# Kernel tuning notes

Measured on AMD Instinct MI355X. Metric: run time of the kernel, lower is better.

The kernel has to match this reference:

```python
import jax, jax.numpy as jnp
import numpy as np

B, T, C = 4, 1024, 768
E, K = 8, 2               # n_exp, top_k
N = B * T                 # num_tokens
# eval-mode capacity: floor(K * eval_capacity(2.0) * N / E), rounded even, >= min_capacity(4)
CAP = 2048


def setup_inputs() -> dict:
    key = jax.random.key(0)
    k0, k1, k2, k3 = jax.random.split(key, 4)
    s = 0.02
    return {
        "x": jax.random.normal(k0, (B, T, C), jnp.float32),
        "w_g": jax.random.normal(k1, (E, C), jnp.float32) * s,
        "c_fc": jax.random.normal(k2, (E, C, 4 * C), jnp.float32) * s,
        "fc_bias": jnp.zeros((E, 1, 4 * C), jnp.float32),
        "c_proj": jax.random.normal(k3, (E, 4 * C, C), jnp.float32) * s,
        "proj_bias": jnp.zeros((E, 1, C), jnp.float32),
    }


def reference(x, w_g, c_fc, fc_bias, c_proj, proj_bias):
    xf = x.reshape(N, C)
    # ---- Router ----
    logits = xf @ w_g.T                                        # [N, E]
    top_v, top_i = jax.lax.top_k(logits, K)                    # [N, K]
    rows = jnp.arange(N)[:, None]
    masked = jnp.full((N, E), -jnp.inf, logits.dtype).at[rows, top_i].set(top_v)
    probs = jax.nn.softmax(masked, axis=-1)                    # [N, E] (zero off top-k)
    exp_mask = jax.nn.one_hot(top_i, E, dtype=jnp.float32)     # [N, K, E]
    exp_mask = exp_mask.transpose(1, 0, 2)                     # [K, N, E]
    # position of each assignment within its expert queue (top-1 assignments first)
    rank = jnp.cumsum(exp_mask.reshape(K * N, E), axis=0) - 1.0
    rank = rank.reshape(K, N, E)
    exp_mask = exp_mask * (rank < CAP)                         # drop over-capacity tokens
    rank_id = jnp.sum(exp_mask * rank, axis=-1).astype(jnp.int32)  # [K, N]
    exp_w = exp_mask * probs[None]                             # [K, N, E]
    rank_sc = jax.nn.one_hot(rank_id, CAP, dtype=jnp.float32)  # [K, N, CAP]
    cb_weight = jnp.einsum('kne,knc->nec', exp_w, rank_sc)     # [N, E, CAP] combine weights
    sec_mask = (cb_weight != 0).astype(xf.dtype)               # [N, E, CAP] dispatch mask
    # ---- Dispatch + batched experts (per-expert MLP via bmm) ----
    exp_in = jnp.einsum('nec,nd->ecd', sec_mask, xf)           # [E, CAP, C]
    h = jax.nn.gelu(jnp.einsum('ecd,edf->ecf', exp_in, c_fc) + fc_bias, approximate=False)
    exp_out = jnp.einsum('ecf,efd->ecd', h, c_proj) + proj_bias  # [E, CAP, C]
    # ---- Combine ----
    out = jnp.einsum('nec,ecd->nd', cb_weight, exp_out)        # [N, C]
    return out.reshape(B, T, C)
```

## Files before the change

### kernel.cpp

```cpp
#include <hip/hip_runtime.h>
#include <hip/hip_bf16.h>
#include <math.h>

#define N_TOK 4096
#define CDIM  768
#define E_EXP 8
#define CAPC  2048
#define HDIM  3072

typedef __attribute__((ext_vector_type(8))) short short8;
typedef __attribute__((ext_vector_type(4))) float floatx4;

#define VMCNT(n) asm volatile("s_waitcnt vmcnt(" #n ")" ::: "memory")
#define LGKM(n)  asm volatile("s_waitcnt lgkmcnt(" #n ")" ::: "memory")
#define SB0()    __builtin_amdgcn_sched_barrier(0)

static __device__ __forceinline__ unsigned short f2bf(float f) {
  __hip_bfloat16 h = __float2bfloat16(f);
  return __builtin_bit_cast(unsigned short, h);
}
static __device__ __forceinline__ float bf2f(unsigned short u) {
  return __builtin_bit_cast(float, (unsigned int)u << 16);
}

__device__ __forceinline__ void transpose_body(const float* __restrict__ ie,
                                               unsigned short* __restrict__ oe,
                                               int R, int Cc, int c0, int r0,
                                               float (*tile)[65])
{
  const int t = threadIdx.x;
  {
    const int r = t >> 2, c = (t & 3) * 4;
#pragma unroll
    for (int i = 0; i < 4; ++i) {
      const float4 v = *(const float4*)(ie + (size_t)(r0 + r) * Cc + c0 + c + i * 16);
      tile[r][c + i * 16 + 0] = v.x; tile[r][c + i * 16 + 1] = v.y;
      tile[r][c + i * 16 + 2] = v.z; tile[r][c + i * 16 + 3] = v.w;
    }
  }
  __syncthreads();
  {
    const int cc = t >> 2, rq = (t & 3) * 16;
    unsigned short o[16];
#pragma unroll
    for (int i = 0; i < 16; ++i) o[i] = f2bf(tile[rq + i][cc]);
    unsigned short* dst = oe + (size_t)(c0 + cc) * R + r0 + rq;
    *(short8*)(dst)     = *(short8*)&o[0];
    *(short8*)(dst + 8) = *(short8*)&o[8];
  }
}

__global__ __launch_bounds__(256)
void prep_kernel(const float* __restrict__ cfc, const float* __restrict__ cpr,
                 __hip_bfloat16* __restrict__ wfcT, __hip_bfloat16* __restrict__ wprT,
                 const float* __restrict__ x, const float* __restrict__ wg,
                 int* __restrict__ eidx, float* __restrict__ pval)
{
  __shared__ float tile[64][65];
  const int b = blockIdx.x;
  if (b < 4608) {
    const int e = b / (48 * 12), rem = b % (48 * 12);
    const int c0 = (rem % 48) * 64, r0 = (rem / 48) * 64;
    transpose_body(cfc + (size_t)e * CDIM * HDIM,
                   (unsigned short*)wfcT + (size_t)e * HDIM * CDIM,
                   CDIM, HDIM, c0, r0, tile);
  } else if (b < 9216) {
    const int bb = b - 4608;
    const int e = bb / (12 * 48), rem = bb % (12 * 48);
    const int c0 = (rem % 12) * 64, r0 = (rem / 12) * 64;
    transpose_body(cpr + (size_t)e * HDIM * CDIM,
                   (unsigned short*)wprT + (size_t)e * CDIM * HDIM,
                   HDIM, CDIM, c0, r0, tile);
  } else {
    const int wv = threadIdx.x >> 6, lane = threadIdx.x & 63;
    const int n = (b - 9216) * 4 + wv;
    const float* xr = x + (size_t)n * CDIM;
    float acc[E_EXP] = {0.f, 0.f, 0.f, 0.f, 0.f, 0.f, 0.f, 0.f};
#pragma unroll
    for (int i = 0; i < CDIM / 64; ++i) {
      const float xv = xr[i * 64 + lane];
#pragma unroll
      for (int e = 0; e < E_EXP; ++e)
        acc[e] = fmaf(xv, wg[e * CDIM + i * 64 + lane], acc[e]);
    }
#pragma unroll
    for (int e = 0; e < E_EXP; ++e) {
#pragma unroll
      for (int off = 32; off > 0; off >>= 1)
        acc[e] += __shfl_xor(acc[e], off);
    }
    if (lane == 0) {
      int e0 = 0; float v0 = acc[0];
#pragma unroll
      for (int e = 1; e < E_EXP; ++e) if (acc[e] > v0) { v0 = acc[e]; e0 = e; }
      int e1 = -1; float v1 = -3.4e38f;
#pragma unroll
      for (int e = 0; e < E_EXP; ++e) if (e != e0 && acc[e] > v1) { v1 = acc[e]; e1 = e; }
      const float ex = __expf(v1 - v0);
      const float inv = 1.f / (1.f + ex);
      eidx[n] = e0; eidx[N_TOK + n] = e1;
      pval[n] = inv; pval[N_TOK + n] = ex * inv;
    }
  }
}

__global__ __launch_bounds__(256)
void scan_kernel(const int* __restrict__ eidx, int* __restrict__ slot,
                 int* __restrict__ slot_token, int* __restrict__ ecnt,
                 int* __restrict__ work2, int* __restrict__ wcnt)
{
  const int t = threadIdx.x;
  const int base = t * 32;
  int e_local[32];
  int cnt[E_EXP] = {0, 0, 0, 0, 0, 0, 0, 0};
#pragma unroll
  for (int i = 0; i < 32; ++i) {
    const int e = eidx[base + i];
    e_local[i] = e;
    cnt[e]++;
  }
  __shared__ int hist[256][E_EXP];
  __shared__ int secnt[E_EXP];
#pragma unroll
  for (int e = 0; e < E_EXP; ++e) hist[t][e] = cnt[e];
  __syncthreads();
  for (int off = 1; off < 256; off <<= 1) {
    int v[E_EXP] = {0, 0, 0, 0, 0, 0, 0, 0};
    if (t >= off) {
#pragma unroll
      for (int e = 0; e < E_EXP; ++e) v[e] = hist[t - off][e];
    }
    __syncthreads();
    if (t >= off) {
#pragma unroll
      for (int e = 0; e < E_EXP; ++e) hist[t][e] += v[e];
    }
    __syncthreads();
  }
  if (t == 255) {
#pragma unroll
    for (int e = 0; e < E_EXP; ++e) {
      const int tot = hist[255][e];
      const int c = tot < CAPC ? tot : CAPC;
      ecnt[e] = c;
      secnt[e] = c;
    }
  }
  __syncthreads();
  if (t == 0) {
    int n2 = 0;
    for (int e = 0; e < E_EXP; ++e) {
      const int c = secnt[e];
      const int t2 = (c + 127) >> 7;
      for (int b = 0; b < t2; ++b) work2[n2++] = (e << 8) | b;
    }
    wcnt[0] = n2 * 24;
    wcnt[1] = n2 * 6;
  }
  int run[E_EXP];
#pragma unroll
  for (int e = 0; e < E_EXP; ++e) run[e] = hist[t][e] - cnt[e];
#pragma unroll
  for (int i = 0; i < 32; ++i) {
    const int a = base + i;
    const int e = e_local[i];
    const int r = run[e]++;
    const int s = (r < CAPC) ? r : -1;
    slot[a] = s;
    if (s >= 0) slot_token[e * CAPC + s] = (a < N_TOK) ? a : (a - N_TOK);
  }
}

__global__ __launch_bounds__(256)
void dispatch_kernel(const float* __restrict__ x, const int* __restrict__ slot_token,
                     const int* __restrict__ ecnt, __hip_bfloat16* __restrict__ xin)
{
  const int wv = threadIdx.x >> 6, lane = threadIdx.x & 63;
  const int s = blockIdx.x * 4 + wv;
  const int e = s >> 11;
  if ((s & (CAPC - 1)) >= ecnt[e]) return;
  const int n = slot_token[s];
  unsigned short* orow = (unsigned short*)xin + (size_t)s * CDIM;
  const float4* xr = (const float4*)(x + (size_t)n * CDIM);
#pragma unroll
  for (int i = 0; i < 3; ++i) {
    const float4 v = xr[i * 64 + lane];
    ushort4 o;
    o.x = f2bf(v.x); o.y = f2bf(v.y); o.z = f2bf(v.z); o.w = f2bf(v.w);
    *(ushort4*)(orow + (size_t)(i * 64 + lane) * 4) = o;
  }
}

__device__ __forceinline__ void stage_ab(const __hip_bfloat16* Ae, const __hip_bfloat16* Be,
                                         char* lds, int K, int kt, int isB,
                                         int wv, int lane)
{
  const char* src = (const char*)(isB ? Be : Ae);
  char* dst = lds + (kt & 1) * 32768 + isB * 16384;
#pragma unroll
  for (int j = 0; j < 4; ++j) {
    const int li = j * 32 + wv * 8 + (lane >> 3);
    const int kb = ((lane & 7) * 16) ^ ((li & 7) << 4);
    const char* g = src + ((size_t)li * K + (size_t)kt * 64) * 2 + kb;
    char* lp = dst + j * 4096 + wv * 1024;
    __builtin_amdgcn_global_load_lds((const __attribute__((address_space(1))) unsigned int*)g,
                                     (__attribute__((address_space(3))) unsigned int*)lp, 16, 0, 0);
  }
}

template<int VME, bool S2>
__device__ __forceinline__ void ktile2(int kt, char* lds,
                                       const __hip_bfloat16* Ae, const __hip_bfloat16* Be,
                                       int K, floatx4 (&acc)[4][4],
                                       int wm, int wn, int fr, int fk, int wv, int lane)
{
  if constexpr (VME == 8) VMCNT(8); else VMCNT(0);
  __builtin_amdgcn_s_barrier();
  SB0();
  const char* bufA = lds + ((kt & 1) ? 32768 : 0);
  const char* bufB = bufA + 16384;
  short8 a[4][2], b[4][2];
#pragma unroll
  for (int mi = 0; mi < 4; ++mi) {
    const int lr = wm * 64 + mi * 16 + fr;
    a[mi][0] = *(const short8*)(bufA + lr * 128 + ((fk * 16) ^ ((lr & 7) << 4)));
  }
#pragma unroll
  for (int ni = 0; ni < 4; ++ni) {
    const int lj = wn * 64 + ni * 16 + fr;
    b[ni][0] = *(const short8*)(bufB + lj * 128 + ((fk * 16) ^ ((lj & 7) << 4)));
  }
  SB0();
#pragma unroll
  for (int mi = 0; mi < 4; ++mi) {
    const int lr = wm * 64 + mi * 16 + fr;
    a[mi][1] = *(const short8*)(bufA + lr * 128 + ((64 + fk * 16) ^ ((lr & 7) << 4)));
  }
#pragma unroll
  for (int ni = 0; ni < 4; ++ni) {
    const int lj = wn * 64 + ni * 16 + fr;
    b[ni][1] = *(const short8*)(bufB + lj * 128 + ((64 + fk * 16) ^ ((lj & 7) << 4)));
  }
  SB0();
  LGKM(8); SB0();
  __builtin_amdgcn_s_setprio(1);
#pragma unroll
  for (int mi = 0; mi < 4; ++mi)
#pragma unroll
    for (int ni = 0; ni < 4; ++ni)
      acc[mi][ni] = __builtin_amdgcn_mfma_f32_16x16x32_bf16(a[mi][0], b[ni][0], acc[mi][ni], 0, 0, 0);
  __builtin_amdgcn_s_setprio(0);
  SB0();
  LGKM(0); SB0();
  __builtin_amdgcn_s_setprio(1);
#pragma unroll
  for (int mi = 0; mi < 4; ++mi)
#pragma unroll
    for (int ni = 0; ni < 4; ++ni)
      acc[mi][ni] = __builtin_amdgcn_mfma_f32_16x16x32_bf16(a[mi][1], b[ni][1], acc[mi][ni], 0, 0, 0);
  __builtin_amdgcn_s_setprio(0);
  SB0();
  __builtin_amdgcn_s_barrier();
  if (S2) {
    stage_ab(Ae, Be, lds, K, kt + 2, 0, wv, lane);
    stage_ab(Ae, Be, lds, K, kt + 2, 1, wv, lane);
  }
  SB0();
}

static __device__ __forceinline__ float gelu_fast(float v) {
  const float u2 = v * (1.5957691216f + 0.0713548163f * v * v);
  const float ez = __expf(u2);
  return v * ez / (ez + 1.0f);
}

template<int EPI>
__device__ __forceinline__ void epilogue_bf16(floatx4 (&acc)[4][4], char* lds,
                                              const float* be, unsigned short* Cb,
                                              int Nn, int m0, int n0,
                                              int wm, int wn, int fr, int fk,
                                              int wv, int lane)
{
  unsigned short* ep = (unsigned short*)(lds + wv * 2048);
  float bcol[4];
#pragma unroll
  for (int ni = 0; ni < 4; ++ni) bcol[ni] = be[n0 + wn * 64 + ni * 16 + fr];
#pragma unroll
  for (int mi = 0; mi < 4; ++mi) {
#pragma unroll
    for (int ni = 0; ni < 4; ++ni)
#pragma unroll
      for (int j = 0; j < 4; ++j) {
        float v = acc[mi][ni][j] + bcol[ni];
        if (EPI == 1) v = gelu_fast(v);
        const int row = fk * 4 + j;
        *(unsigned short*)((char*)ep + row * 128 + ((ni * 32 + fr * 2) ^ (fk << 5))) = f2bf(v);
      }
    LGKM(0); SB0();
    const int r = lane & 15;
    const int grow = m0 + wm * 64 + mi * 16 + r;
#pragma unroll
    for (int it = 0; it < 2; ++it) {
      const int q = (lane >> 4) + it * 4;
      const short8 vv = *(const short8*)((char*)ep + r * 128 + ((q * 16) ^ ((r >> 2) << 5)));
      *(short8*)(Cb + (size_t)grow * Nn + n0 + wn * 64 + q * 8) = vv;
    }
    LGKM(0); SB0();
  }
}

__global__ __launch_bounds__(256, 2)
void gemm1p(const __hip_bfloat16* __restrict__ A, const __hip_bfloat16* __restrict__ Bt,
            const float* __restrict__ bias, __hip_bfloat16* __restrict__ Cout,
            const int* __restrict__ work, const int* __restrict__ wcnt)
{
  extern __shared__ __align__(16) char lds[];
  const int T = wcnt[0];
  const int cpx = (T + 7) >> 3;
  const int x8 = blockIdx.x & 7, l = blockIdx.x >> 3;
  const int lim = (x8 + 1) * cpx < T ? (x8 + 1) * cpx : T;

  const int t = threadIdx.x, wv = t >> 6, lane = t & 63;
  const int wm = wv >> 1, wn = wv & 1;
  const int fr = lane & 15, fk = lane >> 4;
  constexpr int ntk = CDIM / 64;

  for (int i = x8 * cpx + l; i < lim; i += 64) {
    const int p = i / 24;
    const int bx0 = i % 24;
    const int bx = (p & 1) ? (23 - bx0) : bx0;
    const int w = work[p];
    const int e = w >> 8, by = w & 255;

    const __hip_bfloat16* Ae = A + (size_t)e * CAPC * CDIM + (size_t)by * 128 * CDIM;
    const __hip_bfloat16* Be = Bt + (size_t)e * HDIM * CDIM + (size_t)bx * 128 * CDIM;

    floatx4 acc[4][4] = {};

    stage_ab(Ae, Be, lds, CDIM, 0, 0, wv, lane);
    stage_ab(Ae, Be, lds, CDIM, 0, 1, wv, lane);
    stage_ab(Ae, Be, lds, CDIM, 1, 0, wv, lane);
    stage_ab(Ae, Be, lds, CDIM, 1, 1, wv, lane);
    SB0();

#pragma unroll 1
    for (int kt = 0; kt < ntk - 2; ++kt)
      ktile2<8, true>(kt, lds, Ae, Be, CDIM, acc, wm, wn, fr, fk, wv, lane);
    ktile2<8, false>(ntk - 2, lds, Ae, Be, CDIM, acc, wm, wn, fr, fk, wv, lane);
    ktile2<0, false>(ntk - 1, lds, Ae, Be, CDIM, acc, wm, wn, fr, fk, wv, lane);

    epilogue_bf16<1>(acc, lds,
                     bias + (size_t)e * HDIM,
                     (unsigned short*)Cout + (size_t)e * CAPC * HDIM,
                     HDIM, by * 128, bx * 128, wm, wn, fr, fk, wv, lane);
    __builtin_amdgcn_s_barrier();
    SB0();
  }
}

__global__ __launch_bounds__(256, 2)
void gemm2x(const __hip_bfloat16* __restrict__ A, const __hip_bfloat16* __restrict__ Bt,
            const float* __restrict__ bias, __hip_bfloat16* __restrict__ Cout,
            const int* __restrict__ work, const int* __restrict__ wcnt)
{
  extern __shared__ __align__(16) char lds[];
  const int T = wcnt[1];
  const int bId = blockIdx.x;
  const int cpx = (T + 7) >> 3;
  if ((bId >> 3) >= cpx) return;
  const int idx = (bId & 7) * cpx + (bId >> 3);
  if (idx >= T) return;
  const int p = idx / 6;
  const int bx0 = idx % 6;
  const int bx = (p & 1) ? (5 - bx0) : bx0;
  const int w = work[p];
  const int e = w >> 8, by = w & 255;

  const int t = threadIdx.x, wv = t >> 6, lane = t & 63;
  const int wm = wv >> 1, wn = wv & 1;
  const int fr = lane & 15, fk = lane >> 4;
  constexpr int ntk = HDIM / 64;

  const __hip_bfloat16* Ae = A + (size_t)e * CAPC * HDIM + (size_t)by * 128 * HDIM;
  const __hip_bfloat16* Be = Bt + (size_t)e * CDIM * HDIM + (size_t)bx * 128 * HDIM;

  floatx4 acc[4][4] = {};

  stage_ab(Ae, Be, lds, HDIM, 0, 0, wv, lane);
  stage_ab(Ae, Be, lds, HDIM, 0, 1, wv, lane);
  stage_ab(Ae, Be, lds, HDIM, 1, 0, wv, lane);
  stage_ab(Ae, Be, lds, HDIM, 1, 1, wv, lane);
  SB0();

#pragma unroll 1
  for (int kt = 0; kt < ntk - 2; ++kt)
    ktile2<8, true>(kt, lds, Ae, Be, HDIM, acc, wm, wn, fr, fk, wv, lane);
  ktile2<8, false>(ntk - 2, lds, Ae, Be, HDIM, acc, wm, wn, fr, fk, wv, lane);
  ktile2<0, false>(ntk - 1, lds, Ae, Be, HDIM, acc, wm, wn, fr, fk, wv, lane);

  epilogue_bf16<2>(acc, lds,
                   bias + (size_t)e * CDIM,
                   (unsigned short*)Cout + (size_t)e * CAPC * CDIM,
                   CDIM, by * 128, bx * 128, wm, wn, fr, fk, wv, lane);
}

__global__ __launch_bounds__(256)
void combine_kernel(const __hip_bfloat16* __restrict__ eout, const int* __restrict__ eidx,
                    const float* __restrict__ pval, const int* __restrict__ slot,
                    float* __restrict__ out)
{
  const int wv = threadIdx.x >> 6, lane = threadIdx.x & 63;
  const int n = blockIdx.x * 4 + wv;
  const int e0 = eidx[n], e1 = eidx[N_TOK + n];
  int s0 = slot[n], s1 = slot[N_TOK + n];
  const float w0 = (s0 >= 0) ? pval[n] : 0.f;
  const float w1 = (s1 >= 0) ? pval[N_TOK + n] : 0.f;
  s0 = (s0 >= 0) ? s0 : 0;
  s1 = (s1 >= 0) ? s1 : 0;
  const ushort4* r0 = (const ushort4*)((const unsigned short*)eout + ((size_t)e0 * CAPC + s0) * CDIM);
  const ushort4* r1 = (const ushort4*)((const unsigned short*)eout + ((size_t)e1 * CAPC + s1) * CDIM);
  float4* o = (float4*)(out + (size_t)n * CDIM);
#pragma unroll
  for (int i = 0; i < 3; ++i) {
    const ushort4 a = r0[i * 64 + lane];
    const ushort4 b = r1[i * 64 + lane];
    float4 c;
    c.x = w0 * bf2f(a.x) + w1 * bf2f(b.x);
    c.y = w0 * bf2f(a.y) + w1 * bf2f(b.y);
    c.z = w0 * bf2f(a.z) + w1 * bf2f(b.z);
    c.w = w0 * bf2f(a.w) + w1 * bf2f(b.w);
    o[i * 64 + lane] = c;
  }
}

extern "C" void kernel_launch(void* const* d_in, const int* in_sizes, int n_in,
                              void* d_out, int out_size, void* d_ws, size_t ws_size,
                              hipStream_t stream)
{
  const float* x   = (const float*)d_in[0];
  const float* wg  = (const float*)d_in[1];
  const float* cfc = (const float*)d_in[2];
  const float* fcb = (const float*)d_in[3];
  const float* cpr = (const float*)d_in[4];
  const float* prb = (const float*)d_in[5];
  float* out = (float*)d_out;

  char* ws = (char*)d_ws;
  size_t off = 0;
  auto take = [&](size_t bytes) -> void* {
    void* p = ws + off;
    off += (bytes + 255) & ~(size_t)255;
    return p;
  };
  __hip_bfloat16* wfcT = (__hip_bfloat16*)take((size_t)E_EXP * HDIM * CDIM * 2);
  __hip_bfloat16* wprT = (__hip_bfloat16*)take((size_t)E_EXP * CDIM * HDIM * 2);
  __hip_bfloat16* xin  = (__hip_bfloat16*)take((size_t)E_EXP * CAPC * CDIM * 2);
  __hip_bfloat16* hbuf = (__hip_bfloat16*)take((size_t)E_EXP * CAPC * HDIM * 2);
  __hip_bfloat16* eout = (__hip_bfloat16*)take((size_t)E_EXP * CAPC * CDIM * 2);
  int*   eidx = (int*)take((size_t)2 * N_TOK * 4);
  float* pv   = (float*)take((size_t)2 * N_TOK * 4);
  int*   slot = (int*)take((size_t)2 * N_TOK * 4);
  int*   stok = (int*)take((size_t)E_EXP * CAPC * 4);
  int*   ecnt = (int*)take((size_t)E_EXP * 4);
  int*   work2 = (int*)take((size_t)128 * 4);
  int*   wcnt = (int*)take((size_t)2 * 4);

  hipFuncSetAttribute((const void*)gemm1p,
                      hipFuncAttributeMaxDynamicSharedMemorySize, 65536);
  hipFuncSetAttribute((const void*)gemm2x,
                      hipFuncAttributeMaxDynamicSharedMemorySize, 65536);

  prep_kernel<<<4608 + 4608 + 1024, 256, 0, stream>>>(cfc, cpr, wfcT, wprT,
                                                      x, wg, eidx, pv);
  scan_kernel<<<1, 256, 0, stream>>>(eidx, slot, stok, ecnt, work2, wcnt);
  dispatch_kernel<<<(E_EXP * CAPC) / 4, 256, 0, stream>>>(x, stok, ecnt, xin);

  gemm1p<<<512, 256, 65536, stream>>>(xin, wfcT, fcb, hbuf, work2, wcnt);
  gemm2x<<<768, 256, 65536, stream>>>(hbuf, wprT, prb, eout, work2, wcnt);

  combine_kernel<<<N_TOK / 4, 256, 0, stream>>>(eout, eidx, pv, slot, out);
}
```

Measured before the change: 175.4 us.

## Pre-tile transposed expert weights into contiguous per-block K-tiles for GEMM staging

The weight-prep transpose now writes the bf16 weights in a blocked layout: each 128-column by 64-k tile is stored as one contiguous 16 KB chunk, ordered by expert, output block and k-tile. The GEMM B-operand staging reads these chunks linearly instead of striding across rows of K. The prep kernel also uses larger 64x128 tiles, so it launches half as many transpose blocks. The goal is more contiguous global reads in the GEMMs and cheaper prep, at the cost of a more complex layout that both sides must agree on.

```diff
diff --git a/kernel.cpp b/kernel.cpp
--- a/kernel.cpp
+++ b/kernel.cpp
@@ -23,57 +23,57 @@
   return __builtin_bit_cast(float, (unsigned int)u << 16);
 }
 
-__device__ __forceinline__ void transpose_body(const float* __restrict__ ie,
-                                               unsigned short* __restrict__ oe,
-                                               int R, int Cc, int c0, int r0,
-                                               float (*tile)[65])
-{
-  const int t = threadIdx.x;
-  {
-    const int r = t >> 2, c = (t & 3) * 4;
-#pragma unroll
-    for (int i = 0; i < 4; ++i) {
-      const float4 v = *(const float4*)(ie + (size_t)(r0 + r) * Cc + c0 + c + i * 16);
-      tile[r][c + i * 16 + 0] = v.x; tile[r][c + i * 16 + 1] = v.y;
-      tile[r][c + i * 16 + 2] = v.z; tile[r][c + i * 16 + 3] = v.w;
-    }
-  }
-  __syncthreads();
-  {
-    const int cc = t >> 2, rq = (t & 3) * 16;
-    unsigned short o[16];
-#pragma unroll
-    for (int i = 0; i < 16; ++i) o[i] = f2bf(tile[rq + i][cc]);
-    unsigned short* dst = oe + (size_t)(c0 + cc) * R + r0 + rq;
-    *(short8*)(dst)     = *(short8*)&o[0];
-    *(short8*)(dst + 8) = *(short8*)&o[8];
-  }
-}
-
 __global__ __launch_bounds__(256)
 void prep_kernel(const float* __restrict__ cfc, const float* __restrict__ cpr,
                  __hip_bfloat16* __restrict__ wfcT, __hip_bfloat16* __restrict__ wprT,
                  const float* __restrict__ x, const float* __restrict__ wg,
                  int* __restrict__ eidx, float* __restrict__ pval)
 {
-  __shared__ float tile[64][65];
+  __shared__ float tile[64][129];
   const int b = blockIdx.x;
+  const int t = threadIdx.x;
   if (b < 4608) {
-    const int e = b / (48 * 12), rem = b % (48 * 12);
-    const int c0 = (rem % 48) * 64, r0 = (rem / 48) * 64;
-    transpose_body(cfc + (size_t)e * CDIM * HDIM,
-                   (unsigned short*)wfcT + (size_t)e * HDIM * CDIM,
-                   CDIM, HDIM, c0, r0, tile);
-  } else if (b < 9216) {
-    const int bb = b - 4608;
-    const int e = bb / (12 * 48), rem = bb % (12 * 48);
-    const int c0 = (rem % 12) * 64, r0 = (rem / 12) * 64;
-    transpose_body(cpr + (size_t)e * HDIM * CDIM,
-                   (unsigned short*)wprT + (size_t)e * CDIM * HDIM,
-                   HDIM, CDIM, c0, r0, tile);
+    const float* src;
+    unsigned short* dstT;
+    int Cc, bx, kt;
+    if (b < 2304) {
+      const int e = b / 288, rem = b % 288;
+      bx = rem % 24; kt = rem / 24;
+      src = cfc + (size_t)e * CDIM * HDIM;
+      Cc = HDIM;
+      dstT = (unsigned short*)wfcT + ((((size_t)e * 24 + bx) * 12) + kt) * 8192;
+    } else {
+      const int bb = b - 2304;
+      const int e = bb / 288, rem = bb % 288;
+      bx = rem % 6; kt = rem / 6;
+      src = cpr + (size_t)e * HDIM * CDIM;
+      Cc = CDIM;
+      dstT = (unsigned short*)wprT + ((((size_t)e * 6 + bx) * 48) + kt) * 8192;
+    }
+    const float* sbase = src + (size_t)(kt * 64) * Cc + bx * 128;
+#pragma unroll
+    for (int i = 0; i < 8; ++i) {
+      const int r = i * 8 + (t >> 5);
+      const int c = (t & 31) * 4;
+      const float4 v = *(const float4*)(sbase + (size_t)r * Cc + c);
+      tile[r][c + 0] = v.x; tile[r][c + 1] = v.y;
+      tile[r][c + 2] = v.z; tile[r][c + 3] = v.w;
+    }
+    __syncthreads();
+#pragma unroll
+    for (int j = 0; j < 2; ++j) {
+      const int n = j * 64 + (t >> 2);
+      const int kq = (t & 3) * 16;
+      unsigned short o[16];
+#pragma unroll
+      for (int i = 0; i < 16; ++i) o[i] = f2bf(tile[kq + i][n]);
+      unsigned short* d = dstT + n * 64 + kq;
+      *(short8*)(d)     = *(short8*)&o[0];
+      *(short8*)(d + 8) = *(short8*)&o[8];
+    }
   } else {
-    const int wv = threadIdx.x >> 6, lane = threadIdx.x & 63;
-    const int n = (b - 9216) * 4 + wv;
+    const int wv = t >> 6, lane = t & 63;
+    const int n = (b - 4608) * 4 + wv;
     const float* xr = x + (size_t)n * CDIM;
     float acc[E_EXP] = {0.f, 0.f, 0.f, 0.f, 0.f, 0.f, 0.f, 0.f};
 #pragma unroll
@@ -191,26 +191,38 @@
   }
 }
 
-__device__ __forceinline__ void stage_ab(const __hip_bfloat16* Ae, const __hip_bfloat16* Be,
-                                         char* lds, int K, int kt, int isB,
-                                         int wv, int lane)
-{
-  const char* src = (const char*)(isB ? Be : Ae);
-  char* dst = lds + (kt & 1) * 32768 + isB * 16384;
+__device__ __forceinline__ void stage_a(const __hip_bfloat16* Ae, char* lds,
+                                        int K, int kt, int wv, int lane)
+{
+  char* dst = lds + (kt & 1) * 32768;
 #pragma unroll
   for (int j = 0; j < 4; ++j) {
     const int li = j * 32 + wv * 8 + (lane >> 3);
     const int kb = ((lane & 7) * 16) ^ ((li & 7) << 4);
-    const char* g = src + ((size_t)li * K + (size_t)kt * 64) * 2 + kb;
-    char* lp = dst + j * 4096 + wv * 1024;
+    const char* g = (const char*)Ae + ((size_t)li * K + (size_t)kt * 64) * 2 + kb;
     __builtin_amdgcn_global_load_lds((const __attribute__((address_space(1))) unsigned int*)g,
-                                     (__attribute__((address_space(3))) unsigned int*)lp, 16, 0, 0);
+                                     (__attribute__((address_space(3))) unsigned int*)(dst + j * 4096 + wv * 1024),
+                                     16, 0, 0);
+  }
+}
+__device__ __forceinline__ void stage_b(const char* BeT, char* lds,
+                                        int kt, int wv, int lane)
+{
+  char* dst = lds + (kt & 1) * 32768 + 16384;
+#pragma unroll
+  for (int j = 0; j < 4; ++j) {
+    const int li = j * 32 + wv * 8 + (lane >> 3);
+    const int kb = ((lane & 7) * 16) ^ ((li & 7) << 4);
+    const char* g = BeT + (size_t)kt * 16384 + li * 128 + kb;
+    __builtin_amdgcn_global_load_lds((const __attribute__((address_space(1))) unsigned int*)g,
+                                     (__attribute__((address_space(3))) unsigned int*)(dst + j * 4096 + wv * 1024),
+                                     16, 0, 0);
   }
 }
 
 template<int VME, bool S2>
 __device__ __forceinline__ void ktile2(int kt, char* lds,
-                                       const __hip_bfloat16* Ae, const __hip_bfloat16* Be,
+                                       const __hip_bfloat16* Ae, const char* BeT,
                                        int K, floatx4 (&acc)[4][4],
                                        int wm, int wn, int fr, int fk, int wv, int lane)
 {
@@ -262,8 +274,8 @@
   SB0();
   __builtin_amdgcn_s_barrier();
   if (S2) {
-    stage_ab(Ae, Be, lds, K, kt + 2, 0, wv, lane);
-    stage_ab(Ae, Be, lds, K, kt + 2, 1, wv, lane);
+    stage_a(Ae, lds, K, kt + 2, wv, lane);
+    stage_b(BeT, lds, kt + 2, wv, lane);
   }
   SB0();
 }
@@ -333,21 +345,21 @@
     const int e = w >> 8, by = w & 255;
 
     const __hip_bfloat16* Ae = A + (size_t)e * CAPC * CDIM + (size_t)by * 128 * CDIM;
-    const __hip_bfloat16* Be = Bt + (size_t)e * HDIM * CDIM + (size_t)bx * 128 * CDIM;
+    const char* BeT = (const char*)Bt + (((size_t)e * 24 + bx) * 12) * 16384;
 
     floatx4 acc[4][4] = {};
 
-    stage_ab(Ae, Be, lds, CDIM, 0, 0, wv, lane);
-    stage_ab(Ae, Be, lds, CDIM, 0, 1, wv, lane);
-    stage_ab(Ae, Be, lds, CDIM, 1, 0, wv, lane);
-    stage_ab(Ae, Be, lds, CDIM, 1, 1, wv, lane);
+    stage_a(Ae, lds, CDIM, 0, wv, lane);
+    stage_b(BeT, lds, 0, wv, lane);
+    stage_a(Ae, lds, CDIM, 1, wv, lane);
+    stage_b(BeT, lds, 1, wv, lane);
     SB0();
 
 #pragma unroll 1
     for (int kt = 0; kt < ntk - 2; ++kt)
-      ktile2<8, true>(kt, lds, Ae, Be, CDIM, acc, wm, wn, fr, fk, wv, lane);
-    ktile2<8, false>(ntk - 2, lds, Ae, Be, CDIM, acc, wm, wn, fr, fk, wv, lane);
-    ktile2<0, false>(ntk - 1, lds, Ae, Be, CDIM, acc, wm, wn, fr, fk, wv, lane);
+      ktile2<8, true>(kt, lds, Ae, BeT, CDIM, acc, wm, wn, fr, fk, wv, lane);
+    ktile2<8, false>(ntk - 2, lds, Ae, BeT, CDIM, acc, wm, wn, fr, fk, wv, lane);
+    ktile2<0, false>(ntk - 1, lds, Ae, BeT, CDIM, acc, wm, wn, fr, fk, wv, lane);
 
     epilogue_bf16<1>(acc, lds,
                      bias + (size_t)e * HDIM,
@@ -382,21 +394,21 @@
   constexpr int ntk = HDIM / 64;
 
   const __hip_bfloat16* Ae = A + (size_t)e * CAPC * HDIM + (size_t)by * 128 * HDIM;
-  const __hip_bfloat16* Be = Bt + (size_t)e * CDIM * HDIM + (size_t)bx * 128 * HDIM;
+  const char* BeT = (const char*)Bt + (((size_t)e * 6 + bx) * 48) * 16384;
 
   floatx4 acc[4][4] = {};
 
-  stage_ab(Ae, Be, lds, HDIM, 0, 0, wv, lane);
-  stage_ab(Ae, Be, lds, HDIM, 0, 1, wv, lane);
-  stage_ab(Ae, Be, lds, HDIM, 1, 0, wv, lane);
-  stage_ab(Ae, Be, lds, HDIM, 1, 1, wv, lane);
+  stage_a(Ae, lds, HDIM, 0, wv, lane);
+  stage_b(BeT, lds, 0, wv, lane);
+  stage_a(Ae, lds, HDIM, 1, wv, lane);
+  stage_b(BeT, lds, 1, wv, lane);
   SB0();
 
 #pragma unroll 1
   for (int kt = 0; kt < ntk - 2; ++kt)
-    ktile2<8, true>(kt, lds, Ae, Be, HDIM, acc, wm, wn, fr, fk, wv, lane);
-  ktile2<8, false>(ntk - 2, lds, Ae, Be, HDIM, acc, wm, wn, fr, fk, wv, lane);
-  ktile2<0, false>(ntk - 1, lds, Ae, Be, HDIM, acc, wm, wn, fr, fk, wv, lane);
+    ktile2<8, true>(kt, lds, Ae, BeT, HDIM, acc, wm, wn, fr, fk, wv, lane);
+  ktile2<8, false>(ntk - 2, lds, Ae, BeT, HDIM, acc, wm, wn, fr, fk, wv, lane);
+  ktile2<0, false>(ntk - 1, lds, Ae, BeT, HDIM, acc, wm, wn, fr, fk, wv, lane);
 
   epilogue_bf16<2>(acc, lds,
                    bias + (size_t)e * CDIM,
@@ -470,8 +482,7 @@
   hipFuncSetAttribute((const void*)gemm2x,
                       hipFuncAttributeMaxDynamicSharedMemorySize, 65536);
 
-  prep_kernel<<<4608 + 4608 + 1024, 256, 0, stream>>>(cfc, cpr, wfcT, wprT,
-                                                      x, wg, eidx, pv);
+  prep_kernel<<<4608 + 1024, 256, 0, stream>>>(cfc, cpr, wfcT, wprT, x, wg, eidx, pv);
   scan_kernel<<<1, 256, 0, stream>>>(eidx, slot, stok, ecnt, work2, wcnt);
   dispatch_kernel<<<(E_EXP * CAPC) / 4, 256, 0, stream>>>(x, stok, ecnt, xin);
 
```

After: 169.0 us. 1.04x faster.
